# Performance work log

Hardware: AMD Instinct MI355X
Metric: run time of the kernel (lower is better)

The kernel has to match this reference:

```python
import jax, jax.numpy as jnp
import numpy as np

EPS = 1e-12  # matches torch.nn.functional.normalize default eps


def setup_inputs() -> dict:
    key = jax.random.key(0)
    k1, k2 = jax.random.split(key)
    x = jax.random.normal(k1, (2, 32, 64, 128, 128), dtype=jnp.float32)
    gamma = jax.random.normal(k2, (1,), dtype=jnp.float32)
    return {"x": x, "gamma": gamma}


def reference(x, gamma):
    B, N, C, H, W = x.shape
    D = C * H * W
    q = x.reshape(B, N, D)  # proj_query == proj_value == flattened x
    # F.normalize(q, dim=-1): L2 norm per row, clamped to eps.
    # Key is q^T normalized along dim=-2, i.e. same row-normalized q.
    norm = jnp.sqrt(jnp.sum(q * q, axis=-1, keepdims=True))
    qn = q / jnp.maximum(norm, EPS)
    # energy: [B, N, N] cosine-similarity matrix
    energy = jnp.einsum('bnd,bmd->bnm', qn, qn)
    # max-subtract trick (note: max - energy, inverted attention)
    energy_new = jnp.max(energy, axis=-1, keepdims=True) - energy
    attention = jax.nn.softmax(energy_new, axis=-1)
    out = jnp.einsum('bnm,bmd->bnd', attention, q)
    out = out.reshape(B, N, C, H, W)
    out = gamma * out + x
    return out.reshape(B, N * C, H, W)
```

## Files before the change

kernel.cpp:

```cpp
#include <hip/hip_runtime.h>


#define NROW 32
static const size_t D_FULL = 1048576ull;
#define EPSN 1e-12f

typedef __attribute__((ext_vector_type(8)))  __bf16 bf16x8;
typedef __attribute__((ext_vector_type(16))) float  f32x16;

__global__ __launch_bounds__(256) void k_zero(float* g) {
    int i = blockIdx.x * 256 + threadIdx.x;
    ((float4*)g)[i] = make_float4(0.f, 0.f, 0.f, 0.f);
}

__global__ __launch_bounds__(256) void k_gram(const float* __restrict__ x,
                                              float* __restrict__ gpart) {
    const int tid  = threadIdx.x;
    const int w    = tid >> 6;
    const int lane = tid & 63;
    const int b    = blockIdx.x >> 8;
    const int dblk = (blockIdx.x & 255) << 12;
    const int row  = lane & 31;
    const int kg   = lane >> 5;

    const float* p = x + ((size_t)(b * NROW + row)) * D_FULL
                       + (size_t)dblk + (size_t)w * 1024 + (size_t)kg * 8;

    f32x16 acc = (f32x16)(0.0f);
    #pragma unroll 4
    for (int it = 0; it < 64; ++it) {
        float4 v0 = *(const float4*)(p);
        float4 v1 = *(const float4*)(p + 4);
        bf16x8 f;
        f[0] = (__bf16)v0.x; f[1] = (__bf16)v0.y;
        f[2] = (__bf16)v0.z; f[3] = (__bf16)v0.w;
        f[4] = (__bf16)v1.x; f[5] = (__bf16)v1.y;
        f[6] = (__bf16)v1.z; f[7] = (__bf16)v1.w;
        acc = __builtin_amdgcn_mfma_f32_32x32x16_bf16(f, f, acc, 0, 0, 0);
        p += 16;
    }

    __shared__ float red[4][1024];
    const int col  = lane & 31;
    const int rsel = lane >> 5;
    #pragma unroll
    for (int r = 0; r < 16; ++r) {
        int rw = (r & 3) + 8 * (r >> 2) + 4 * rsel;
        red[w][rw * 32 + col] = acc[r];
    }
    __syncthreads();

    float* dst = gpart + (size_t)(blockIdx.x & 7) * 2048 + (size_t)b * 1024;
    for (int e = tid; e < 1024; e += 256) {
        float s = red[0][e] + red[1][e] + red[2][e] + red[3][e];
        atomicAdd(&dst[e], s);
    }
}

__global__ __launch_bounds__(1024) void k_attn(const float* __restrict__ gpart,
                                               const float* __restrict__ gamma_p,
                                               float* __restrict__ M) {
    const int b   = blockIdx.x;
    const int tid = threadIdx.x;
    const int n   = tid >> 5;
    const int m   = tid & 31;

    float g = 0.f;
    #pragma unroll
    for (int s = 0; s < 8; ++s) g += gpart[(size_t)s * 2048 + (size_t)b * 1024 + tid];

    __shared__ float nrm[32];
    if (n == m) nrm[n] = fmaxf(sqrtf(g), EPSN);
    __syncthreads();

    float e = g / (nrm[n] * nrm[m]);

    float rmax = e, rmin = e;
    #pragma unroll
    for (int off = 16; off > 0; off >>= 1) {
        rmax = fmaxf(rmax, __shfl_xor(rmax, off, 32));
        rmin = fminf(rmin, __shfl_xor(rmin, off, 32));
    }
    float pv  = expf(rmin - e);
    float sum = pv;
    #pragma unroll
    for (int off = 16; off > 0; off >>= 1) sum += __shfl_xor(sum, off, 32);
    float a = pv / sum;

    float gm = gamma_p[0];
    M[(size_t)b * 1024 + tid] = gm * a + (n == m ? 1.f : 0.f);
}

__device__ __forceinline__ void fma4(float4& o, float c, const float4& a) {
    o.x += c * a.x; o.y += c * a.y; o.z += c * a.z; o.w += c * a.w;
}

__global__ __launch_bounds__(256) void k_apply(const float* __restrict__ x,
                                               const float* __restrict__ M,
                                               float* __restrict__ out) {
    __shared__ __align__(16) float Ml[1024];
    const int tid = threadIdx.x;
    const int b   = blockIdx.x >> 10;
    const float* Mb = M + (size_t)b * 1024;
    #pragma unroll
    for (int i = 0; i < 4; ++i) Ml[tid + i * 256] = Mb[tid + i * 256];
    __syncthreads();

    const size_t d4   = ((size_t)(blockIdx.x & 1023)) * 256 + tid;
    const size_t rs4  = D_FULL / 4;
    const float4* xb  = (const float4*)(x)   + (size_t)b * NROW * rs4;
    float4*       ob  = (float4*)(out)       + (size_t)b * NROW * rs4;

    float4 qv[32];
    #pragma unroll
    for (int m = 0; m < 32; ++m) qv[m] = xb[(size_t)m * rs4 + d4];

    for (int n = 0; n < 32; ++n) {
        const float4* Mr = (const float4*)(&Ml[n * 32]);
        float4 o = make_float4(0.f, 0.f, 0.f, 0.f);
        #pragma unroll
        for (int m4 = 0; m4 < 8; ++m4) {
            float4 c = Mr[m4];
            fma4(o, c.x, qv[m4 * 4 + 0]);
            fma4(o, c.y, qv[m4 * 4 + 1]);
            fma4(o, c.z, qv[m4 * 4 + 2]);
            fma4(o, c.w, qv[m4 * 4 + 3]);
        }
        ob[(size_t)n * rs4 + d4] = o;
    }
}

extern "C" void kernel_launch(void* const* d_in, const int* in_sizes, int n_in,
                              void* d_out, int out_size, void* d_ws, size_t ws_size,
                              hipStream_t stream) {
    const float* x     = (const float*)d_in[0];
    const float* gamma = (const float*)d_in[1];
    float*       out   = (float*)d_out;
    float*       ws    = (float*)d_ws;

    float* gpart = ws;
    float* Mws   = ws + 16384;

    k_zero <<<16,   256,  0, stream>>>(gpart);
    k_gram <<<512,  256,  0, stream>>>(x, gpart);
    k_attn <<<2,    1024, 0, stream>>>(gpart, gamma, Mws);
    k_apply<<<2048, 256,  0, stream>>>(x, Mws, out);
}
```

Baseline: 596.0 us.

## Stage Gram tiles through LDS with coalesced loads, more blocks, nontemporal output stores

```diff
diff --git a/kernel.cpp b/kernel.cpp
--- a/kernel.cpp
+++ b/kernel.cpp
@@ -6,41 +6,58 @@
 #define EPSN 1e-12f
 
 typedef __attribute__((ext_vector_type(8)))  __bf16 bf16x8;
+typedef __attribute__((ext_vector_type(4)))  __bf16 bf16x4;
 typedef __attribute__((ext_vector_type(16))) float  f32x16;
+typedef __attribute__((ext_vector_type(4)))  float  f32x4;
 
 __global__ __launch_bounds__(256) void k_zero(float* g) {
     int i = blockIdx.x * 256 + threadIdx.x;
     ((float4*)g)[i] = make_float4(0.f, 0.f, 0.f, 0.f);
 }
 
-__global__ __launch_bounds__(256) void k_gram(const float* __restrict__ x,
-                                              float* __restrict__ gpart) {
+#define GSTRIDE 520
+__global__ __launch_bounds__(256, 4) void k_gram(const float* __restrict__ x,
+                                                 float* __restrict__ gpart) {
+    __shared__ __align__(16) unsigned char smem[NROW * GSTRIDE * 2];
+    __bf16* tile = (__bf16*)smem;
+    float (*red)[1024] = (float (*)[1024])smem;
+
     const int tid  = threadIdx.x;
     const int w    = tid >> 6;
     const int lane = tid & 63;
-    const int b    = blockIdx.x >> 8;
-    const int dblk = (blockIdx.x & 255) << 12;
+    const int b    = (int)(blockIdx.x >> 9);
+    const size_t dblk = ((size_t)(blockIdx.x & 511)) * 2048;
     const int row  = lane & 31;
     const int kg   = lane >> 5;
 
-    const float* p = x + ((size_t)(b * NROW + row)) * D_FULL
-                       + (size_t)dblk + (size_t)w * 1024 + (size_t)kg * 8;
+    const float* xb = x + (size_t)b * NROW * D_FULL + dblk;
+    const int srow0 = tid >> 7;
+    const int sc4   = tid & 127;
 
     f32x16 acc = (f32x16)(0.0f);
-    #pragma unroll 4
-    for (int it = 0; it < 64; ++it) {
-        float4 v0 = *(const float4*)(p);
-        float4 v1 = *(const float4*)(p + 4);
-        bf16x8 f;
-        f[0] = (__bf16)v0.x; f[1] = (__bf16)v0.y;
-        f[2] = (__bf16)v0.z; f[3] = (__bf16)v0.w;
-        f[4] = (__bf16)v1.x; f[5] = (__bf16)v1.y;
-        f[6] = (__bf16)v1.z; f[7] = (__bf16)v1.w;
-        acc = __builtin_amdgcn_mfma_f32_32x32x16_bf16(f, f, acc, 0, 0, 0);
-        p += 16;
+
+    for (int s = 0; s < 4; ++s) {
+        __syncthreads();
+        const float* src = xb + s * 512;
+        #pragma unroll
+        for (int sw = 0; sw < 16; ++sw) {
+            int r = sw * 2 + srow0;
+            float4 v = *(const float4*)(src + (size_t)r * D_FULL + sc4 * 4);
+            bf16x4 h;
+            h[0] = (__bf16)v.x; h[1] = (__bf16)v.y;
+            h[2] = (__bf16)v.z; h[3] = (__bf16)v.w;
+            *(bf16x4*)&tile[r * GSTRIDE + sc4 * 4] = h;
+        }
+        __syncthreads();
+        #pragma unroll
+        for (int kk = 0; kk < 8; ++kk) {
+            int kstep = w * 8 + kk;
+            bf16x8 f = *(const bf16x8*)&tile[row * GSTRIDE + kstep * 16 + kg * 8];
+            acc = __builtin_amdgcn_mfma_f32_32x32x16_bf16(f, f, acc, 0, 0, 0);
+        }
     }
+    __syncthreads();
 
-    __shared__ float red[4][1024];
     const int col  = lane & 31;
     const int rsel = lane >> 5;
     #pragma unroll
@@ -52,8 +69,8 @@
 
     float* dst = gpart + (size_t)(blockIdx.x & 7) * 2048 + (size_t)b * 1024;
     for (int e = tid; e < 1024; e += 256) {
-        float s = red[0][e] + red[1][e] + red[2][e] + red[3][e];
-        atomicAdd(&dst[e], s);
+        float sum = red[0][e] + red[1][e] + red[2][e] + red[3][e];
+        atomicAdd(&dst[e], sum);
     }
 }
 
@@ -75,20 +92,16 @@
 
     float e = g / (nrm[n] * nrm[m]);
 
-    float rmax = e, rmin = e;
+    float rmin = e;
     #pragma unroll
-    for (int off = 16; off > 0; off >>= 1) {
-        rmax = fmaxf(rmax, __shfl_xor(rmax, off, 32));
-        rmin = fminf(rmin, __shfl_xor(rmin, off, 32));
-    }
+    for (int off = 16; off > 0; off >>= 1) rmin = fminf(rmin, __shfl_xor(rmin, off, 32));
     float pv  = expf(rmin - e);
     float sum = pv;
     #pragma unroll
     for (int off = 16; off > 0; off >>= 1) sum += __shfl_xor(sum, off, 32);
     float a = pv / sum;
 
-    float gm = gamma_p[0];
-    M[(size_t)b * 1024 + tid] = gm * a + (n == m ? 1.f : 0.f);
+    M[(size_t)b * 1024 + tid] = gamma_p[0] * a + (n == m ? 1.f : 0.f);
 }
 
 __device__ __forceinline__ void fma4(float4& o, float c, const float4& a) {
@@ -106,10 +119,10 @@
     for (int i = 0; i < 4; ++i) Ml[tid + i * 256] = Mb[tid + i * 256];
     __syncthreads();
 
-    const size_t d4   = ((size_t)(blockIdx.x & 1023)) * 256 + tid;
-    const size_t rs4  = D_FULL / 4;
-    const float4* xb  = (const float4*)(x)   + (size_t)b * NROW * rs4;
-    float4*       ob  = (float4*)(out)       + (size_t)b * NROW * rs4;
+    const size_t d4  = ((size_t)(blockIdx.x & 1023)) * 256 + tid;
+    const size_t rs4 = D_FULL / 4;
+    const float4* xb = (const float4*)(x) + (size_t)b * NROW * rs4;
+    f32x4*        ob = (f32x4*)(out)      + (size_t)b * NROW * rs4;
 
     float4 qv[32];
     #pragma unroll
@@ -126,7 +139,8 @@
             fma4(o, c.z, qv[m4 * 4 + 2]);
             fma4(o, c.w, qv[m4 * 4 + 3]);
         }
-        ob[(size_t)n * rs4 + d4] = o;
+        f32x4 ov; ov[0] = o.x; ov[1] = o.y; ov[2] = o.z; ov[3] = o.w;
+        __builtin_nontemporal_store(ov, &ob[(size_t)n * rs4 + d4]);
     }
 }
 
@@ -142,7 +156,7 @@
     float* Mws   = ws + 16384;
 
     k_zero <<<16,   256,  0, stream>>>(gpart);
-    k_gram <<<512,  256,  0, stream>>>(x, gpart);
+    k_gram <<<1024, 256,  0, stream>>>(x, gpart);
     k_attn <<<2,    1024, 0, stream>>>(gpart, gamma, Mws);
     k_apply<<<2048, 256,  0, stream>>>(x, Mws, out);
 }
```

After: 524.3 us. 12.0% less time.
